# Optimization experiments

Hardware: AMD Instinct MI355X
Metric: run time of the kernel (lower is better)

Reference implementation:

```python
import jax, jax.numpy as jnp
import numpy as np

ALPHA = 0.2  # leaky relu slope


def _gat(h, W, b, a_src, a_dst, a_b):
    # h: [B,T,Din]; W: [H,Din,C]; b,a_src,a_dst: [H,C]; a_b: [H]
    Wh = jnp.einsum('btd,hdc->bhtc', h, W) + b[None, :, None, :]
    src = jnp.einsum('bhtc,hc->bht', Wh, a_src)  # score from Wh_i half of concat
    dst = jnp.einsum('bhtc,hc->bht', Wh, a_dst)  # score from Wh_j half
    e = src[:, :, :, None] + dst[:, :, None, :] + a_b[None, :, None, None]  # [B,H,T,T]
    e = jnp.where(e >= 0, e, ALPHA * e)  # leaky_relu
    a = jax.nn.softmax(e, axis=-1)
    out = jnp.einsum('bhij,bhjc->bhic', a, Wh)
    out = jax.nn.relu(out)  # last=False branch
    B, H, T, C = out.shape
    out = out.transpose(0, 2, 1, 3).reshape(B, T, H * C)  # concat heads on feature dim
    return jax.nn.sigmoid(out)


def setup_inputs() -> dict:
    key = jax.random.key(0)
    ks = jax.random.split(key, 15)
    B, T, D = 16, 128, 256
    H, C1, C2, OUT_W = 64, 64, 20, 32
    s = lambda k, shape, fan: jax.random.normal(k, shape, jnp.float32) * (1.0 / np.sqrt(fan))
    return {
        'x': jax.random.normal(ks[0], (B, T, D), jnp.float32),
        'W1': s(ks[1], (H, D, C1), D), 'b1': s(ks[2], (H, C1), D),
        'a1s': s(ks[3], (H, C1), 2 * C1), 'a1d': s(ks[4], (H, C1), 2 * C1),
        'a1b': s(ks[5], (H,), 2 * C1),
        'W2': s(ks[6], (H, H * C1, C2), H * C1), 'b2': s(ks[7], (H, C2), H * C1),
        'a2s': s(ks[8], (H, C2), 2 * C2), 'a2d': s(ks[9], (H, C2), 2 * C2),
        'a2b': s(ks[10], (H,), 2 * C2),
        'sl_w': s(ks[11], (H * C2, D), H * C2), 'sl_b': s(ks[12], (D,), H * C2),
        'gar_w': s(ks[13], (T, OUT_W), T), 'gar_b': s(ks[14], (OUT_W,), T),
    }


def reference(x, W1, b1, a1s, a1d, a1b, W2, b2, a2s, a2d, a2b, sl_w, sl_b, gar_w, gar_b):
    c = _gat(x, W1, b1, a1s, a1d, a1b)          # [B,T,H*C1]
    c = jax.nn.relu(c)
    c = _gat(c, W2, b2, a2s, a2d, a2b)          # [B,T,H*C2]
    c = c @ sl_w + sl_b                          # [B,T,D]
    # GAR: linear over time dim: [B,T,D] -> [B,OUT_W,D]
    res = jnp.einsum('btd,to->bod', c, gar_w) + gar_b[None, :, None]
    return res
```

## Files before the change

### kernel.cpp

```cpp
#include <hip/hip_runtime.h>
#include <hip/hip_bf16.h>

#define B 16
#define T 128
#define D 256
#define H 64
#define C1 64
#define C2 20
#define K2 4096
#define F2 1280
#define OUTW 32
#define ALPHA 0.2f

typedef __attribute__((ext_vector_type(8))) short short8;
typedef __attribute__((ext_vector_type(4))) float f32x4;

static __device__ __forceinline__ ushort f2bf(float f) {
    __hip_bfloat16 h = __float2bfloat16(f);
    return *reinterpret_cast<ushort*>(&h);
}
static __device__ __forceinline__ float bf2f(ushort u) {
    return __uint_as_float(((unsigned int)u) << 16);
}
static __device__ __forceinline__ void gload16(const ushort* g, ushort* l) {
    __builtin_amdgcn_global_load_lds((const unsigned int*)g, (unsigned int*)l,
                                     16, 0, 0);
}

template<int KD, int NBLK, int MBLK, int KSPLIT, int PERM>
__global__ __launch_bounds__(256) void gemm_splitk_kernel(
    const ushort* __restrict__ Ag, const ushort* __restrict__ Bg,
    ushort* __restrict__ Cp)
{
    __shared__ ushort As[128 * 64];
    __shared__ ushort Bs[128 * 64];
    constexpr int NN = NBLK * 128;
    constexpr int MM = MBLK * 128;
    constexpr int NT = MBLK * NBLK;
    constexpr int TOTAL = NT * KSPLIT;
    constexpr int KDP = KD / KSPLIT;
    static_assert(TOTAL % 8 == 0, "swizzle needs multiple of 8 blocks");

    int tid = threadIdx.x;
    int bid = blockIdx.x;
    int wg = (bid & 7) * (TOTAL / 8) + (bid >> 3);
    int kp = wg / NT; int tile = wg - kp * NT;
    int bm = (tile / NBLK) * 128, bn = (tile % NBLK) * 128;

    int wave = tid >> 6, lane = tid & 63;
    int wm = (wave >> 1) * 64, wn = (wave & 1) * 64;
    int lr = lane & 15, lk = lane >> 4;
    int srow = lane >> 3, scol = (lane & 7) * 8;

    f32x4 acc[4][4];
    #pragma unroll
    for (int i = 0; i < 4; ++i)
        #pragma unroll
        for (int j = 0; j < 4; ++j) acc[i][j] = (f32x4){0.f, 0.f, 0.f, 0.f};

    const ushort* ApB = Ag + (size_t)bm * KD + kp * KDP;
    const ushort* BpB = Bg + (size_t)bn * KD + kp * KDP;

    for (int k0 = 0; k0 < KDP; k0 += 64) {
        __syncthreads();
        #pragma unroll
        for (int e = 0; e < 4; ++e) {
            int c = e * 4 + wave;
            gload16(ApB + (size_t)(8 * c + srow) * KD + k0 + scol, &As[c * 512]);
            gload16(BpB + (size_t)(8 * c + srow) * KD + k0 + scol, &Bs[c * 512]);
        }
        __syncthreads();
        #pragma unroll
        for (int ks = 0; ks < 2; ++ks) {
            short8 af[4], bfr[4];
            #pragma unroll
            for (int i = 0; i < 4; ++i)
                af[i] = *(const short8*)&As[(wm + i * 16 + lr) * 64 + ks * 32 + lk * 8];
            #pragma unroll
            for (int j = 0; j < 4; ++j)
                bfr[j] = *(const short8*)&Bs[(wn + j * 16 + lr) * 64 + ks * 32 + lk * 8];
            #pragma unroll
            for (int i = 0; i < 4; ++i)
                #pragma unroll
                for (int j = 0; j < 4; ++j)
                    acc[i][j] = __builtin_amdgcn_mfma_f32_16x16x32_bf16(
                        af[i], bfr[j], acc[i][j], 0, 0, 0);
        }
    }

    if constexpr (PERM) {
        ushort* Cw = Cp + (size_t)kp * MM * NN + (size_t)tile * 16384
                   + wave * 4096 + lane * 4;
        #pragma unroll
        for (int i = 0; i < 4; ++i)
            #pragma unroll
            for (int j = 0; j < 4; ++j) {
                union { ushort q[4]; uint2 v; } pk;
                #pragma unroll
                for (int r = 0; r < 4; ++r) pk.q[r] = f2bf(acc[i][j][r]);
                *(uint2*)&Cw[(i * 4 + j) * 256] = pk.v;
            }
    } else {
        ushort* Cout = Cp + (size_t)kp * MM * NN;
        #pragma unroll
        for (int i = 0; i < 4; ++i) {
            #pragma unroll
            for (int j = 0; j < 4; ++j) {
                int col = bn + wn + j * 16 + lr;
                #pragma unroll
                for (int r = 0; r < 4; ++r) {
                    int row = bm + wm + i * 16 + lk * 4 + r;
                    Cout[(size_t)row * NN + col] = f2bf(acc[i][j][r]);
                }
            }
        }
    }
}

template<int P, int NN>
__global__ __launch_bounds__(256) void reduce_bias_kernel(
    const ushort* __restrict__ parts, const float* __restrict__ bias,
    float* __restrict__ out, int MN)
{
    size_t off = ((size_t)blockIdx.x * 256 + threadIdx.x) * 4;
    float s0 = 0.f, s1 = 0.f, s2 = 0.f, s3 = 0.f;
    #pragma unroll
    for (int p = 0; p < P; ++p) {
        uint2 v = *(const uint2*)&parts[(size_t)p * MN + off];
        s0 += bf2f((ushort)(v.x & 0xffff));
        s1 += bf2f((ushort)(v.x >> 16));
        s2 += bf2f((ushort)(v.y & 0xffff));
        s3 += bf2f((ushort)(v.y >> 16));
    }
    float4 bv = *(const float4*)&bias[(int)(off % NN)];
    float4 o; o.x = s0 + bv.x; o.y = s1 + bv.y; o.z = s2 + bv.z; o.w = s3 + bv.w;
    *(float4*)&out[off] = o;
}

#define WHT_(r,c) whT[(r) * 136 + (c)]

__global__ __launch_bounds__(256) void fused1_kernel(
    const ushort* __restrict__ xbf,
    const ushort* __restrict__ w1t,
    const float* __restrict__ b1,
    const float* __restrict__ a1s, const float* __restrict__ a1d,
    const float* __restrict__ a1b,
    ushort* __restrict__ c1)
{
    int blk = blockIdx.x; int b = blk >> 6, h = blk & 63;
    __shared__ ushort whT[64 * 136];
    __shared__ ushort CT[128 * 72];
    __shared__ float ss[128], ddv[128], sinv[128];

    int tid = threadIdx.x;
    int wave = tid >> 6, lane = tid & 63;
    int wm2 = wave * 32;
    int lr = lane & 15, lk = lane >> 4;

    f32x4 acc[2][4];
    #pragma unroll
    for (int i = 0; i < 2; ++i)
        #pragma unroll
        for (int j = 0; j < 4; ++j) acc[i][j] = (f32x4){0.f, 0.f, 0.f, 0.f};

    const ushort* Abase = xbf + (size_t)(b * T + wm2 + lr) * D + lk * 8;
    const ushort* Bbase = w1t + (size_t)(h * 64 + lr) * D + lk * 8;

    #pragma unroll 2
    for (int kb = 0; kb < 8; ++kb) {
        short8 af[2], bfr[4];
        #pragma unroll
        for (int i = 0; i < 2; ++i)
            af[i] = *(const short8*)(Abase + (size_t)i * 16 * D + kb * 32);
        #pragma unroll
        for (int j = 0; j < 4; ++j)
            bfr[j] = *(const short8*)(Bbase + (size_t)j * 16 * D + kb * 32);
        #pragma unroll
        for (int i = 0; i < 2; ++i)
            #pragma unroll
            for (int j = 0; j < 4; ++j)
                acc[i][j] = __builtin_amdgcn_mfma_f32_16x16x32_bf16(
                    af[i], bfr[j], acc[i][j], 0, 0, 0);
    }

    #pragma unroll
    for (int j = 0; j < 4; ++j) {
        int col = j * 16 + lr;
        float bv = b1[h * C1 + col];
        #pragma unroll
        for (int i = 0; i < 2; ++i) {
            int t0 = wm2 + i * 16 + lk * 4;
            union { ushort q[4]; uint2 v; } pk;
            #pragma unroll
            for (int r = 0; r < 4; ++r) pk.q[r] = f2bf(acc[i][j][r] + bv);
            *(uint2*)&WHT_(col, t0) = pk.v;
        }
    }
    __syncthreads();

    {
        int t = tid & 127;
        bool isS = tid < 128;
        const float* av = (isS ? a1s : a1d) + h * C1;
        float s = isS ? a1b[h] : 0.f;
        #pragma unroll 8
        for (int c = 0; c < 64; ++c) s = fmaf(bf2f(WHT_(c, t)), av[c], s);
        if (isS) ss[t] = s; else ddv[t] = s;
    }
    __syncthreads();

    float dm = fmaxf(ddv[lane], ddv[lane + 64]);
    #pragma unroll
    for (int msk = 1; msk < 64; msk <<= 1) dm = fmaxf(dm, __shfl_xor(dm, msk));

    float si[2], mi[2], rsum[2];
    #pragma unroll
    for (int i = 0; i < 2; ++i) {
        si[i] = ss[wm2 + i * 16 + lr];
        float mx = si[i] + dm;
        mi[i] = mx >= 0.f ? mx : ALPHA * mx;
        rsum[i] = 0.f;
    }

    f32x4 acc2[2][4];
    #pragma unroll
    for (int i = 0; i < 2; ++i)
        #pragma unroll
        for (int j = 0; j < 4; ++j) acc2[i][j] = (f32x4){0.f, 0.f, 0.f, 0.f};

    #pragma unroll
    for (int ks = 0; ks < 4; ++ks) {
        float dj[8];
        #pragma unroll
        for (int e = 0; e < 8; ++e) dj[e] = ddv[ks * 32 + lk * 8 + e];
        short8 bfr[4];
        #pragma unroll
        for (int j = 0; j < 4; ++j)
            bfr[j] = *(const short8*)&WHT_(j * 16 + lr, ks * 32 + lk * 8);
        #pragma unroll
        for (int i = 0; i < 2; ++i) {
            union { ushort q[8]; short8 s; } pk;
            #pragma unroll
            for (int e = 0; e < 8; ++e) {
                float ee = si[i] + dj[e];
                ee = ee >= 0.f ? ee : ALPHA * ee;
                float pp = __expf(ee - mi[i]);
                rsum[i] += pp;
                pk.q[e] = f2bf(pp);
            }
            #pragma unroll
            for (int j = 0; j < 4; ++j)
                acc2[i][j] = __builtin_amdgcn_mfma_f32_16x16x32_bf16(
                    pk.s, bfr[j], acc2[i][j], 0, 0, 0);
        }
    }

    #pragma unroll
    for (int i = 0; i < 2; ++i) {
        rsum[i] += __shfl_xor(rsum[i], 16);
        rsum[i] += __shfl_xor(rsum[i], 32);
    }
    if (lk == 0) {
        #pragma unroll
        for (int i = 0; i < 2; ++i) sinv[wm2 + i * 16 + lr] = 1.0f / rsum[i];
    }
    __syncthreads();

    #pragma unroll
    for (int i = 0; i < 2; ++i) {
        #pragma unroll
        for (int r = 0; r < 4; ++r) {
            int row = wm2 + i * 16 + lk * 4 + r;
            float sv = sinv[row];
            #pragma unroll
            for (int j = 0; j < 4; ++j) {
                int col = j * 16 + lr;
                float v = acc2[i][j][r] * sv;
                v = v > 0.f ? v : 0.f;
                v = 1.0f / (1.0f + __expf(-v));
                CT[row * 72 + col] = f2bf(v);
            }
        }
    }
    __syncthreads();
    #pragma unroll
    for (int e = 0; e < 4; ++e) {
        int idx = e * 256 + tid;
        int row = idx >> 3, q = idx & 7;
        uint4 v = *(const uint4*)&CT[row * 72 + q * 8];
        *(uint4*)&c1[((size_t)(b * T + row)) * K2 + h * C1 + q * 8] = v;
    }
}

#define PB2_(r,c)  Pb2[(r) * 136 + (c)]
#define WHT2_(r,c) whT2[(r) * 136 + (c)]

__global__ __launch_bounds__(256) void fused2_kernel(
    const ushort* __restrict__ wh2pb,
    const float* __restrict__ b2,
    const float* __restrict__ a2s, const float* __restrict__ a2d,
    const float* __restrict__ a2b,
    ushort* __restrict__ c2)
{
    int blk = blockIdx.x; int b = blk >> 6, h = blk & 63;
    __shared__ ushort Pb2[128 * 136];
    __shared__ ushort whT2[32 * 136];
    __shared__ float ss[128], ddv[128], sinv[128];

    int tid = threadIdx.x;
    int wave = tid >> 6, lane = tid & 63;
    int lr = lane & 15, lk = lane >> 4;
    const size_t MNfull = (size_t)2048 * F2;

    for (int e = 0; e < 3; ++e) {
        int idx = e * 256 + tid;
        if (idx < 640) {
            int tq = idx / 20, c = idx - tq * 20;
            int col = h * C2 + c;
            int tn = col >> 7, cl = col & 127;
            int fj = (cl >> 4) & 3, fl = cl & 15;
            int t0 = tq * 4;
            int wv = ((t0 >> 6) << 1) | (cl >> 6);
            int fi = (t0 >> 4) & 3, fk = (t0 >> 2) & 3;
            size_t fa = (size_t)(b * 10 + tn) * 16384 + wv * 4096
                      + (fi * 4 + fj) * 256 + (fk * 16 + fl) * 4;
            float bv = b2[col];
            float s0 = bv, s1 = bv, s2 = bv, s3 = bv;
            #pragma unroll
            for (int p = 0; p < 8; ++p) {
                uint2 v = *(const uint2*)&wh2pb[p * MNfull + fa];
                s0 += bf2f((ushort)(v.x & 0xffff));
                s1 += bf2f((ushort)(v.x >> 16));
                s2 += bf2f((ushort)(v.y & 0xffff));
                s3 += bf2f((ushort)(v.y >> 16));
            }
            union { ushort q[4]; uint2 u; } o;
            o.q[0] = f2bf(s0); o.q[1] = f2bf(s1);
            o.q[2] = f2bf(s2); o.q[3] = f2bf(s3);
            *(uint2*)&WHT2_(c, t0) = o.u;
        }
    }
    {
        int idx = tid;
        for (int e = 0; e < 6; ++e, idx += 256) {
            int c = 20 + (idx >> 7), t = idx & 127;
            WHT2_(c, t) = 0;
        }
    }
    __syncthreads();

    {
        int t = tid & 127;
        bool isS = tid < 128;
        const float* av = (isS ? a2s : a2d) + h * C2;
        float s = isS ? a2b[h] : 0.f;
        #pragma unroll
        for (int c = 0; c < 20; ++c) s = fmaf(bf2f(WHT2_(c, t)), av[c], s);
        if (isS) ss[t] = s; else ddv[t] = s;
    }
    __syncthreads();

    {
        float dm = fmaxf(ddv[lane], ddv[lane + 64]);
        #pragma unroll
        for (int msk = 1; msk < 64; msk <<= 1) dm = fmaxf(dm, __shfl_xor(dm, msk));
        int i = tid >> 1, j0 = (tid & 1) * 64;
        float si = ss[i];
        float mx = si + dm; mx = mx >= 0.f ? mx : ALPHA * mx;
        float lsum = 0.f;
        #pragma unroll
        for (int g = 0; g < 8; ++g) {
            union { ushort q[8]; uint4 v; } pk;
            #pragma unroll
            for (int e = 0; e < 8; ++e) {
                float ee = si + ddv[j0 + g * 8 + e];
                ee = ee >= 0.f ? ee : ALPHA * ee;
                float pp = __expf(ee - mx);
                lsum += pp;
                pk.q[e] = f2bf(pp);
            }
            *(uint4*)&PB2_(i, j0 + g * 8) = pk.v;
        }
        lsum += __shfl_xor(lsum, 1);
        if (!(tid & 1)) sinv[i] = 1.0f / lsum;
    }
    __syncthreads();

    int wm2 = wave * 32;
    f32x4 acc2[2][2];
    #pragma unroll
    for (int i = 0; i < 2; ++i)
        #pragma unroll
        for (int j = 0; j < 2; ++j) acc2[i][j] = (f32x4){0.f, 0.f, 0.f, 0.f};

    #pragma unroll
    for (int ks = 0; ks < 4; ++ks) {
        short8 af[2], bfr[2];
        #pragma unroll
        for (int i = 0; i < 2; ++i)
            af[i] = *(const short8*)&PB2_(wm2 + i * 16 + lr, ks * 32 + lk * 8);
        #pragma unroll
        for (int j = 0; j < 2; ++j)
            bfr[j] = *(const short8*)&WHT2_(j * 16 + lr, ks * 32 + lk * 8);
        #pragma unroll
        for (int i = 0; i < 2; ++i)
            #pragma unroll
            for (int j = 0; j < 2; ++j)
                acc2[i][j] = __builtin_amdgcn_mfma_f32_16x16x32_bf16(
                    af[i], bfr[j], acc2[i][j], 0, 0, 0);
    }

    __syncthreads();
    ushort* CT2 = Pb2;
    #pragma unroll
    for (int i = 0; i < 2; ++i) {
        #pragma unroll
        for (int r = 0; r < 4; ++r) {
            int row = wm2 + i * 16 + lk * 4 + r;
            float sv = sinv[row];
            #pragma unroll
            for (int j = 0; j < 2; ++j) {
                int col = j * 16 + lr;
                if (col < C2) {
                    float v = acc2[i][j][r] * sv;
                    v = v > 0.f ? v : 0.f;
                    v = 1.0f / (1.0f + __expf(-v));
                    CT2[row * 24 + col] = f2bf(v);
                }
            }
        }
    }
    __syncthreads();
    for (int e = 0; e < 3; ++e) {
        int idx = e * 256 + tid;
        if (idx < 640) {
            int row = idx / 5, q = idx - row * 5;
            uint2 v = *(const uint2*)&CT2[row * 24 + q * 4];
            *(uint2*)&c2[((size_t)(b * T + row)) * F2 + h * C2 + q * 4] = v;
        }
    }
}

__global__ __launch_bounds__(256) void xbf_kernel(
    const float* __restrict__ x, ushort* __restrict__ xbf)
{
    int i = blockIdx.x * 256 + threadIdx.x;
    float4 v = *(const float4*)&x[(size_t)i * 4];
    union { ushort u[4]; uint2 p; } o;
    o.u[0] = f2bf(v.x); o.u[1] = f2bf(v.y);
    o.u[2] = f2bf(v.z); o.u[3] = f2bf(v.w);
    *(uint2*)&xbf[(size_t)i * 4] = o.p;
}

__global__ __launch_bounds__(256) void w1t_kernel(
    const float* __restrict__ W1, ushort* __restrict__ w1t)
{
    int blk = blockIdx.x; int h = blk >> 2, d0 = (blk & 3) * 64;
    __shared__ float lw[64][65];
    int tid = threadIdx.x;
    for (int e = 0; e < 16; ++e) {
        int idx = e * 256 + tid; int dr = idx >> 6, c = idx & 63;
        lw[dr][c] = W1[((size_t)h * D + d0 + dr) * C1 + c];
    }
    __syncthreads();
    for (int e = 0; e < 16; ++e) {
        int idx = e * 256 + tid; int c = idx >> 6, dr = idx & 63;
        w1t[((size_t)(h * 64 + c)) * D + d0 + dr] = f2bf(lw[dr][c]);
    }
}

__global__ __launch_bounds__(256) void w2t_kernel(
    const float* __restrict__ W2, ushort* __restrict__ w2t)
{
    int blk = blockIdx.x; int h = blk >> 5, kb = blk & 31; int k0 = kb * 128;
    __shared__ float lw[128][21];
    int tid = threadIdx.x;
    const float* src = W2 + ((size_t)h * K2 + k0) * C2;
    for (int e = 0; e < 10; ++e) {
        int idx = e * 256 + tid; int k = idx / 20, c = idx - k * 20;
        lw[k][c] = src[idx];
    }
    __syncthreads();
    for (int e = 0; e < 10; ++e) {
        int idx = e * 256 + tid; int c = idx >> 7, k = idx & 127;
        w2t[((size_t)(h * 20 + c)) * K2 + k0 + k] = f2bf(lw[k][c]);
    }
}

__global__ __launch_bounds__(256) void slwt_kernel(
    const float* __restrict__ slw, ushort* __restrict__ slwt)
{
    int blk = blockIdx.x; int kb = blk >> 2, d0 = (blk & 3) * 64; int k0 = kb * 64;
    __shared__ float lw[64][65];
    int tid = threadIdx.x;
    for (int e = 0; e < 16; ++e) {
        int idx = e * 256 + tid; int kr = idx >> 6, dc = idx & 63;
        lw[kr][dc] = slw[((size_t)(k0 + kr)) * D + d0 + dc];
    }
    __syncthreads();
    for (int e = 0; e < 16; ++e) {
        int idx = e * 256 + tid; int dr = idx >> 6, kc = idx & 63;
        slwt[((size_t)(d0 + dr)) * F2 + k0 + kc] = f2bf(lw[kc][dr]);
    }
}

__global__ __launch_bounds__(256) void gar_kernel(
    const float* __restrict__ c3, const float* __restrict__ garw,
    const float* __restrict__ garb, float* __restrict__ out)
{
    int blk = blockIdx.x; int b = blk >> 5, o = blk & 31;
    int dcol = threadIdx.x;
    float acc = garb[o];
    const float* cp = c3 + (size_t)b * T * D + dcol;
    for (int t = 0; t < T; ++t)
        acc = fmaf(cp[(size_t)t * D], garw[t * OUTW + o], acc);
    out[((size_t)b * OUTW + o) * D + dcol] = acc;
}

extern "C" void kernel_launch(void* const* d_in, const int* in_sizes, int n_in,
                              void* d_out, int out_size, void* d_ws, size_t ws_size,
                              hipStream_t stream) {
    const float* x    = (const float*)d_in[0];
    const float* W1   = (const float*)d_in[1];
    const float* b1   = (const float*)d_in[2];
    const float* a1s  = (const float*)d_in[3];
    const float* a1d  = (const float*)d_in[4];
    const float* a1b  = (const float*)d_in[5];
    const float* W2   = (const float*)d_in[6];
    const float* b2   = (const float*)d_in[7];
    const float* a2s  = (const float*)d_in[8];
    const float* a2d  = (const float*)d_in[9];
    const float* a2b  = (const float*)d_in[10];
    const float* slw  = (const float*)d_in[11];
    const float* slb  = (const float*)d_in[12];
    const float* garw = (const float*)d_in[13];
    const float* garb = (const float*)d_in[14];

    char* p = (char*)d_ws;
    float*  c3    = (float*)p;   p += (size_t)2048 * 256  * 4;
    ushort* xbf   = (ushort*)p;  p += (size_t)2048 * 256  * 2;
    ushort* w1t   = (ushort*)p;  p += (size_t)4096 * 256  * 2;
    ushort* c1bf  = (ushort*)p;  p += (size_t)2048 * 4096 * 2;
    ushort* w2t   = (ushort*)p;  p += (size_t)1280 * 4096 * 2;
    ushort* c2bf  = (ushort*)p;  p += (size_t)2048 * 1280 * 2;
    ushort* slwt  = (ushort*)p;  p += (size_t)256  * 1280 * 2;
    ushort* wh2pb = (ushort*)p;  p += (size_t)8 * 2048 * 1280 * 2;
    ushort* c3pb  = (ushort*)c1bf;

    xbf_kernel <<<512,  256, 0, stream>>>(x, xbf);
    w1t_kernel <<<256,  256, 0, stream>>>(W1, w1t);
    w2t_kernel <<<2048, 256, 0, stream>>>(W2, w2t);
    slwt_kernel<<<80,   256, 0, stream>>>(slw, slwt);

    fused1_kernel<<<B * H, 256, 0, stream>>>(xbf, w1t, b1, a1s, a1d, a1b, c1bf);

    gemm_splitk_kernel<4096, 10, 16, 8, 1><<<1280, 256, 0, stream>>>(c1bf, w2t,
                                                                     wh2pb);
    fused2_kernel<<<B * H, 256, 0, stream>>>(wh2pb, b2, a2s, a2d, a2b, c2bf);

    gemm_splitk_kernel<1280, 2, 16, 4, 0><<<128, 256, 0, stream>>>(c2bf, slwt,
                                                                   c3pb);
    reduce_bias_kernel<4, 256><<<512, 256, 0, stream>>>(c3pb, slb, c3, 2048 * 256);

    gar_kernel<<<B * OUTW, 256, 0, stream>>>(c3, garw, garb, (float*)d_out);
}
```

Before: 124.1 us.

## Merge prep kernels into one launch and fuse split-K reduce with GAR

The four weight and input conversion kernels become one prep kernel that dispatches on block index ranges, which removes three launches. The split-K partial reduce plus bias is folded into a new GAR kernel that sums the bf16 partials straight into shared memory and computes the time-dimension linear from LDS, register-blocked over 8 outputs. This drops the fp32 c3 intermediate and one more launch. The new GAR runs only 64 blocks, so it uses little of the GPU's parallelism, and the shared-memory union raises LDS use for the small x-conversion blocks.

```diff
diff --git a/kernel.cpp b/kernel.cpp
--- a/kernel.cpp
+++ b/kernel.cpp
@@ -115,26 +115,6 @@
             }
         }
     }
-}
-
-template<int P, int NN>
-__global__ __launch_bounds__(256) void reduce_bias_kernel(
-    const ushort* __restrict__ parts, const float* __restrict__ bias,
-    float* __restrict__ out, int MN)
-{
-    size_t off = ((size_t)blockIdx.x * 256 + threadIdx.x) * 4;
-    float s0 = 0.f, s1 = 0.f, s2 = 0.f, s3 = 0.f;
-    #pragma unroll
-    for (int p = 0; p < P; ++p) {
-        uint2 v = *(const uint2*)&parts[(size_t)p * MN + off];
-        s0 += bf2f((ushort)(v.x & 0xffff));
-        s1 += bf2f((ushort)(v.x >> 16));
-        s2 += bf2f((ushort)(v.y & 0xffff));
-        s3 += bf2f((ushort)(v.y >> 16));
-    }
-    float4 bv = *(const float4*)&bias[(int)(off % NN)];
-    float4 o; o.x = s0 + bv.x; o.y = s1 + bv.y; o.z = s2 + bv.z; o.w = s3 + bv.w;
-    *(float4*)&out[off] = o;
 }
 
 #define WHT_(r,c) whT[(r) * 136 + (c)]
@@ -441,80 +421,99 @@
     }
 }
 
-__global__ __launch_bounds__(256) void xbf_kernel(
-    const float* __restrict__ x, ushort* __restrict__ xbf)
+__global__ __launch_bounds__(256) void prep_kernel(
+    const float* __restrict__ x,  const float* __restrict__ W1,
+    const float* __restrict__ W2, const float* __restrict__ slw,
+    ushort* __restrict__ xbf, ushort* __restrict__ w1t,
+    ushort* __restrict__ w2t, ushort* __restrict__ slwt)
 {
-    int i = blockIdx.x * 256 + threadIdx.x;
-    float4 v = *(const float4*)&x[(size_t)i * 4];
-    union { ushort u[4]; uint2 p; } o;
-    o.u[0] = f2bf(v.x); o.u[1] = f2bf(v.y);
-    o.u[2] = f2bf(v.z); o.u[3] = f2bf(v.w);
-    *(uint2*)&xbf[(size_t)i * 4] = o.p;
-}
-
-__global__ __launch_bounds__(256) void w1t_kernel(
-    const float* __restrict__ W1, ushort* __restrict__ w1t)
-{
-    int blk = blockIdx.x; int h = blk >> 2, d0 = (blk & 3) * 64;
-    __shared__ float lw[64][65];
-    int tid = threadIdx.x;
-    for (int e = 0; e < 16; ++e) {
-        int idx = e * 256 + tid; int dr = idx >> 6, c = idx & 63;
-        lw[dr][c] = W1[((size_t)h * D + d0 + dr) * C1 + c];
-    }
-    __syncthreads();
-    for (int e = 0; e < 16; ++e) {
-        int idx = e * 256 + tid; int c = idx >> 6, dr = idx & 63;
-        w1t[((size_t)(h * 64 + c)) * D + d0 + dr] = f2bf(lw[dr][c]);
-    }
-}
-
-__global__ __launch_bounds__(256) void w2t_kernel(
-    const float* __restrict__ W2, ushort* __restrict__ w2t)
-{
-    int blk = blockIdx.x; int h = blk >> 5, kb = blk & 31; int k0 = kb * 128;
-    __shared__ float lw[128][21];
-    int tid = threadIdx.x;
-    const float* src = W2 + ((size_t)h * K2 + k0) * C2;
-    for (int e = 0; e < 10; ++e) {
-        int idx = e * 256 + tid; int k = idx / 20, c = idx - k * 20;
-        lw[k][c] = src[idx];
-    }
-    __syncthreads();
-    for (int e = 0; e < 10; ++e) {
-        int idx = e * 256 + tid; int c = idx >> 7, k = idx & 127;
-        w2t[((size_t)(h * 20 + c)) * K2 + k0 + k] = f2bf(lw[k][c]);
-    }
-}
-
-__global__ __launch_bounds__(256) void slwt_kernel(
-    const float* __restrict__ slw, ushort* __restrict__ slwt)
-{
-    int blk = blockIdx.x; int kb = blk >> 2, d0 = (blk & 3) * 64; int k0 = kb * 64;
-    __shared__ float lw[64][65];
-    int tid = threadIdx.x;
-    for (int e = 0; e < 16; ++e) {
-        int idx = e * 256 + tid; int kr = idx >> 6, dc = idx & 63;
-        lw[kr][dc] = slw[((size_t)(k0 + kr)) * D + d0 + dc];
-    }
-    __syncthreads();
-    for (int e = 0; e < 16; ++e) {
-        int idx = e * 256 + tid; int dr = idx >> 6, kc = idx & 63;
-        slwt[((size_t)(d0 + dr)) * F2 + k0 + kc] = f2bf(lw[kc][dr]);
-    }
-}
-
-__global__ __launch_bounds__(256) void gar_kernel(
-    const float* __restrict__ c3, const float* __restrict__ garw,
+    __shared__ union { float a[64][65]; float b[128][21]; } lw;
+    int bid = blockIdx.x, tid = threadIdx.x;
+
+    if (bid < 512) {
+        int i = bid * 256 + tid;
+        float4 v = *(const float4*)&x[(size_t)i * 4];
+        union { ushort u[4]; uint2 p; } o;
+        o.u[0] = f2bf(v.x); o.u[1] = f2bf(v.y);
+        o.u[2] = f2bf(v.z); o.u[3] = f2bf(v.w);
+        *(uint2*)&xbf[(size_t)i * 4] = o.p;
+    } else if (bid < 768) {
+        int blk = bid - 512; int h = blk >> 2, d0 = (blk & 3) * 64;
+        for (int e = 0; e < 16; ++e) {
+            int idx = e * 256 + tid; int dr = idx >> 6, c = idx & 63;
+            lw.a[dr][c] = W1[((size_t)h * D + d0 + dr) * C1 + c];
+        }
+        __syncthreads();
+        for (int e = 0; e < 16; ++e) {
+            int idx = e * 256 + tid; int c = idx >> 6, dr = idx & 63;
+            w1t[((size_t)(h * 64 + c)) * D + d0 + dr] = f2bf(lw.a[dr][c]);
+        }
+    } else if (bid < 2816) {
+        int blk = bid - 768; int h = blk >> 5, kb = blk & 31; int k0 = kb * 128;
+        const float* src = W2 + ((size_t)h * K2 + k0) * C2;
+        for (int e = 0; e < 10; ++e) {
+            int idx = e * 256 + tid; int k = idx / 20, c = idx - k * 20;
+            lw.b[k][c] = src[idx];
+        }
+        __syncthreads();
+        for (int e = 0; e < 10; ++e) {
+            int idx = e * 256 + tid; int c = idx >> 7, k = idx & 127;
+            w2t[((size_t)(h * 20 + c)) * K2 + k0 + k] = f2bf(lw.b[k][c]);
+        }
+    } else {
+        int blk = bid - 2816; int kb = blk >> 2, d0 = (blk & 3) * 64;
+        int k0 = kb * 64;
+        for (int e = 0; e < 16; ++e) {
+            int idx = e * 256 + tid; int kr = idx >> 6, dc = idx & 63;
+            lw.a[kr][dc] = slw[((size_t)(k0 + kr)) * D + d0 + dc];
+        }
+        __syncthreads();
+        for (int e = 0; e < 16; ++e) {
+            int idx = e * 256 + tid; int dr = idx >> 6, kc = idx & 63;
+            slwt[((size_t)(d0 + dr)) * F2 + k0 + kc] = f2bf(lw.a[kc][dr]);
+        }
+    }
+}
+
+__global__ __launch_bounds__(256) void gar2_kernel(
+    const ushort* __restrict__ c3pb,
+    const float* __restrict__ slb, const float* __restrict__ garw,
     const float* __restrict__ garb, float* __restrict__ out)
 {
-    int blk = blockIdx.x; int b = blk >> 5, o = blk & 31;
-    int dcol = threadIdx.x;
-    float acc = garb[o];
-    const float* cp = c3 + (size_t)b * T * D + dcol;
-    for (int t = 0; t < T; ++t)
-        acc = fmaf(cp[(size_t)t * D], garw[t * OUTW + o], acc);
-    out[((size_t)b * OUTW + o) * D + dcol] = acc;
+    int blk = blockIdx.x; int b = blk >> 2, dt = (blk & 3) * 64;
+    __shared__ float cs[128][65];
+    __shared__ float gw[128][32];
+    int tid = threadIdx.x;
+
+    for (int e = 0; e < 32; ++e) {
+        int idx = e * 256 + tid;
+        int t = idx >> 6, d = idx & 63;
+        size_t off = (size_t)(b * T + t) * D + dt + d;
+        float s = slb[dt + d];
+        #pragma unroll
+        for (int p = 0; p < 4; ++p)
+            s += bf2f(c3pb[(size_t)p * 2048 * 256 + off]);
+        cs[t][d] = s;
+    }
+    for (int e = 0; e < 16; ++e) {
+        int idx = e * 256 + tid;
+        int t = idx >> 5, o = idx & 31;
+        gw[t][o] = garw[t * OUTW + o];
+    }
+    __syncthreads();
+
+    int d = tid & 63, o0 = (tid >> 6) * 8;
+    float accv[8];
+    #pragma unroll
+    for (int q = 0; q < 8; ++q) accv[q] = garb[o0 + q];
+    for (int t = 0; t < T; ++t) {
+        float cv = cs[t][d];
+        #pragma unroll
+        for (int q = 0; q < 8; ++q) accv[q] = fmaf(cv, gw[t][o0 + q], accv[q]);
+    }
+    #pragma unroll
+    for (int q = 0; q < 8; ++q)
+        out[((size_t)b * OUTW + o0 + q) * D + dt + d] = accv[q];
 }
 
 extern "C" void kernel_launch(void* const* d_in, const int* in_sizes, int n_in,
@@ -537,7 +536,6 @@
     const float* garb = (const float*)d_in[14];
 
     char* p = (char*)d_ws;
-    float*  c3    = (float*)p;   p += (size_t)2048 * 256  * 4;
     ushort* xbf   = (ushort*)p;  p += (size_t)2048 * 256  * 2;
     ushort* w1t   = (ushort*)p;  p += (size_t)4096 * 256  * 2;
     ushort* c1bf  = (ushort*)p;  p += (size_t)2048 * 4096 * 2;
@@ -547,10 +545,7 @@
     ushort* wh2pb = (ushort*)p;  p += (size_t)8 * 2048 * 1280 * 2;
     ushort* c3pb  = (ushort*)c1bf;
 
-    xbf_kernel <<<512,  256, 0, stream>>>(x, xbf);
-    w1t_kernel <<<256,  256, 0, stream>>>(W1, w1t);
-    w2t_kernel <<<2048, 256, 0, stream>>>(W2, w2t);
-    slwt_kernel<<<80,   256, 0, stream>>>(slw, slwt);
+    prep_kernel<<<2896, 256, 0, stream>>>(x, W1, W2, slw, xbf, w1t, w2t, slwt);
 
     fused1_kernel<<<B * H, 256, 0, stream>>>(xbf, w1t, b1, a1s, a1d, a1b, c1bf);
 
@@ -560,7 +555,6 @@
 
     gemm_splitk_kernel<1280, 2, 16, 4, 0><<<128, 256, 0, stream>>>(c2bf, slwt,
                                                                    c3pb);
-    reduce_bias_kernel<4, 256><<<512, 256, 0, stream>>>(c3pb, slb, c3, 2048 * 256);
-
-    gar_kernel<<<B * OUTW, 256, 0, stream>>>(c3, garw, garb, (float*)d_out);
-}
+    gar2_kernel<<<B * 4, 256, 0, stream>>>(c3pb, slb, garw, garb,
+                                           (float*)d_out);
+}
```

Result: faster. 114.4 us (-7.8%).
